# Kernel tuning notes

Measured on AMD Instinct MI355X. Metric: run time of the kernel, lower is better.

Reference implementation:

```python
import jax, jax.numpy as jnp
import numpy as np

VOCAB = 50000
EMB = 512
HID = 1024
B = 256
W = 26


def setup_inputs() -> dict:
    key = jax.random.key(0)
    k0, k1, k2, k3, k4, k5, k6 = jax.random.split(key, 7)
    s = 1.0 / np.sqrt(HID)
    return {
        "ques_vec": jax.random.randint(k0, (B, W), 0, VOCAB + 1, dtype=jnp.int32),
        "ques_len": jax.random.randint(k1, (B,), 1, W + 1, dtype=jnp.int32),
        # nn.Linear(vocab, emb, bias=False).weight -> [emb, vocab]
        "W_emb": jax.random.normal(k2, (EMB, VOCAB), dtype=jnp.float32) * 0.02,
        # PyTorch LSTM params, gate order (i, f, g, o)
        "W_ih": jax.random.uniform(k3, (4 * HID, EMB), jnp.float32, -s, s),
        "W_hh": jax.random.uniform(k4, (4 * HID, HID), jnp.float32, -s, s),
        "b_ih": jax.random.uniform(k5, (4 * HID,), jnp.float32, -s, s),
        "b_hh": jax.random.uniform(k6, (4 * HID,), jnp.float32, -s, s),
    }


def reference(ques_vec, ques_len, W_emb, W_ih, W_hh, b_ih, b_hh):
    # one_hot(vocab+1)[:, :, 1:] @ W_emb.T  ==  gather of W_emb columns;
    # token 0 (pad) maps to the zero embedding.
    tok = ques_vec  # [B, W]
    emb = jnp.where(
        (tok > 0)[..., None],
        W_emb.T[jnp.maximum(tok - 1, 0)],  # [B, W, EMB]
        jnp.zeros((), dtype=W_emb.dtype),
    )
    emb = jnp.tanh(emb)  # tanh(0)=0 for pads, matches torch

    bias = b_ih + b_hh

    def step(carry, xt):
        h, c = carry
        gates = xt @ W_ih.T + h @ W_hh.T + bias  # [B, 4H]
        i, f, g, o = jnp.split(gates, 4, axis=-1)
        c = jax.nn.sigmoid(f) * c + jax.nn.sigmoid(i) * jnp.tanh(g)
        h = jax.nn.sigmoid(o) * jnpp_tanh(c) if False else jax.nn.sigmoid(o) * jnp.tanh(c)
        return (h, c), None

    h0 = jnp.zeros((tok.shape[0], HID), dtype=W_emb.dtype)
    (h_n, _), _ = jax.lax.scan(step, (h0, h0), jnp.swapaxes(emb, 0, 1))
    return h_n  # [B, HID] == h_n.view(B, -1) for 1-layer unidirectional LSTM
```

## Files before the change

### kernel.cpp

```cpp
#include <hip/hip_runtime.h>
#include <hip/hip_bf16.h>

#define VOCAB 50000
#define EMBD  512
#define HID   1024
#define NB    256
#define SEQW  26
#define MTOT  (SEQW * NB)
#define NGATE (4 * HID)

typedef short short8 __attribute__((ext_vector_type(8)));
typedef _Float16 half8 __attribute__((ext_vector_type(8)));
typedef float f32x4  __attribute__((ext_vector_type(4)));
typedef float f32x2  __attribute__((ext_vector_type(2)));

__device__ __forceinline__ unsigned short f16bits(_Float16 h) {
    union { _Float16 h; unsigned short u; } cv; cv.h = h; return cv.u;
}

__device__ __forceinline__ void gload16(const void* g, void* l) {
    __builtin_amdgcn_global_load_lds(
        (const __attribute__((address_space(1))) void*)g,
        (__attribute__((address_space(3))) void*)l, 16, 0, 0);
}

__global__ void init_kernel(unsigned short* __restrict__ hBuf,
                            unsigned int* __restrict__ bar) {
    int idx = blockIdx.x * blockDim.x + threadIdx.x;
    hBuf[idx] = 0;
    if (idx < 4096) bar[idx] = 0;
}

__global__ void transp_kernel(const float* __restrict__ W,
                              unsigned short* __restrict__ WT) {
    __shared__ _Float16 tile[64][72];
    int v0 = blockIdx.x * 64;
    int e0 = blockIdx.y * 64;
    int tid = threadIdx.x;

    int e_loc = tid >> 2, q = tid & 3;
    int vq = q * 16;
    if (v0 + vq < VOCAB) {
        const float* src = W + (size_t)(e0 + e_loc) * VOCAB + v0 + vq;
        #pragma unroll
        for (int j = 0; j < 4; ++j) {
            f32x4 x = *(const f32x4*)(src + 4 * j);
            #pragma unroll
            for (int i = 0; i < 4; ++i)
                tile[vq + 4 * j + i][e_loc] = (_Float16)x[i];
        }
    }
    __syncthreads();

    int v_loc = tid >> 2;
    int ec = q * 16;
    int v = v0 + v_loc;
    if (v < VOCAB) {
        short8* dst = (short8*)(WT + (size_t)v * EMBD + e0 + ec);
        dst[0] = *(const short8*)&tile[v_loc][ec];
        dst[1] = *(const short8*)&tile[v_loc][ec + 8];
    }
}

__global__ void embed_kernel(const int* __restrict__ qv,
                             const unsigned short* __restrict__ WT,
                             unsigned short* __restrict__ eHi) {
    int pair = blockIdx.x * 4 + (threadIdx.x >> 6);
    int t = pair >> 8, b = pair & 255;
    int lane = threadIdx.x & 63;
    int tok = qv[b * SEQW + t];
    short8 out = {};
    if (tok > 0) {
        short8 v = *(const short8*)(WT + (size_t)(tok - 1) * EMBD + lane * 8);
        #pragma unroll
        for (int i = 0; i < 8; ++i) {
            union { short s; _Float16 h; } cv; cv.s = v[i];
            out[i] = (short)f16bits((_Float16)tanhf((float)cv.h));
        }
    }
    *(short8*)(eHi + (size_t)pair * EMBD + lane * 8) = out;
}

__global__ void convw_kernel(const float* __restrict__ Wih,
                             const float* __restrict__ Whh,
                             const float* __restrict__ b_ih,
                             const float* __restrict__ b_hh,
                             unsigned short* __restrict__ ih,
                             unsigned short* __restrict__ hh,
                             float* __restrict__ bsum) {
    int j = blockIdx.x;
    if (threadIdx.x == 0) bsum[j] = b_ih[j] + b_hh[j];
    for (int col = threadIdx.x; col < EMBD; col += blockDim.x)
        ih[(size_t)j * EMBD + col] = f16bits((_Float16)Wih[(size_t)j * EMBD + col]);
    for (int col = threadIdx.x; col < HID; col += blockDim.x)
        hh[(size_t)j * HID + col] = f16bits((_Float16)Whh[(size_t)j * HID + col]);
}

__global__ __launch_bounds__(512, 2) void pregemm_kernel(
    const unsigned short* __restrict__ eHi,
    const unsigned short* __restrict__ ih,
    const float* __restrict__ bsum,
    float* __restrict__ G0n)
{
    __shared__ char smem[65536];

    int id = blockIdx.x;
    int xcd = id & 7, lid = id >> 3;
    int pc = xcd * 4 + (lid & 3);
    int pm = lid >> 2;
    int m0 = pm * 128;

    int tid = threadIdx.x;
    int w = tid >> 6;
    int mh = w >> 2, nh = w & 3;
    int lane = tid & 63;
    int col16 = lane & 15, g4 = lane >> 4;

    int sr = lane >> 3, sc = lane & 7;
    int ra0 = w * 16 + sr, ra1 = ra0 + 8;
    const char* eB = (const char*)eHi;
    const char* iB = (const char*)ih;
    size_t aOffG0 = (size_t)(m0 + ra0) * 1024 + (size_t)(((sc ^ (ra0 & 7))) * 16);
    size_t aOffG1 = (size_t)(m0 + ra1) * 1024 + (size_t)(((sc ^ (ra1 & 7))) * 16);
    int gb0 = (ra0 >> 5) * 1024 + pc * 32 + (ra0 & 31);
    int gb1 = (ra1 >> 5) * 1024 + pc * 32 + (ra1 & 31);
    size_t bOffG0 = (size_t)gb0 * 1024 + (size_t)(((sc ^ (ra0 & 7))) * 16);
    size_t bOffG1 = (size_t)gb1 * 1024 + (size_t)(((sc ^ (ra1 & 7))) * 16);
    int ldsRow0 = (w * 16) * 128;
    int ldsRow1 = (w * 16 + 8) * 128;

    f32x4 acc[4][2];
    #pragma unroll
    for (int fm = 0; fm < 4; ++fm)
        #pragma unroll
        for (int fn = 0; fn < 2; ++fn)
            acc[fm][fn] = (f32x4){0.f, 0.f, 0.f, 0.f};

    int swb = col16 & 7;
    int aRow[4], bRow[2];
    #pragma unroll
    for (int fm = 0; fm < 4; ++fm) aRow[fm] = (mh * 64 + fm * 16 + col16) * 128;
    #pragma unroll
    for (int fn = 0; fn < 2; ++fn) bRow[fn] = (nh * 32 + fn * 16 + col16) * 128;

#define STAGE(kb, buf) do { \
        int kby = (kb) * 128; \
        char* aD = smem + (buf) * 16384; \
        char* bD = smem + 32768 + (buf) * 16384; \
        gload16(eB + aOffG0 + kby, aD + ldsRow0); \
        gload16(eB + aOffG1 + kby, aD + ldsRow1); \
        gload16(iB + bOffG0 + kby, bD + ldsRow0); \
        gload16(iB + bOffG1 + kby, bD + ldsRow1); \
    } while (0)

    STAGE(0, 0);
    #pragma unroll
    for (int kb = 0; kb < 8; ++kb) {
        int cur = kb & 1;
        __syncthreads();
        if (kb < 7) STAGE(kb + 1, cur ^ 1);
        const char* aS = smem + cur * 16384;
        const char* bS = smem + 32768 + cur * 16384;
        #pragma unroll
        for (int kk = 0; kk < 2; ++kk) {
            int co = ((kk * 4 + g4) ^ swb) * 16;
            half8 bF[2];
            #pragma unroll
            for (int fn = 0; fn < 2; ++fn)
                bF[fn] = *(const half8*)(const void*)(bS + bRow[fn] + co);
            #pragma unroll
            for (int fm = 0; fm < 4; ++fm) {
                half8 aF = *(const half8*)(const void*)(aS + aRow[fm] + co);
                #pragma unroll
                for (int fn = 0; fn < 2; ++fn)
                    acc[fm][fn] = __builtin_amdgcn_mfma_f32_16x16x32_f16(
                        aF, bF[fn], acc[fm][fn], 0, 0, 0);
            }
        }
    }
#undef STAGE

    #pragma unroll
    for (int fn = 0; fn < 2; ++fn) {
        int cp = nh * 32 + fn * 16 + col16;
        int gate = cp >> 5;
        int jh = pc * 32 + (cp & 31);
        int ct = jh >> 4, jl = jh & 15;
        int cidx = gate * 16 + jl;
        float bv = bsum[gate * HID + jh];
        #pragma unroll
        for (int fm = 0; fm < 4; ++fm)
            #pragma unroll
            for (int r = 0; r < 4; ++r) {
                int row = m0 + mh * 64 + fm * 16 + g4 * 4 + r;
                int t = row >> 8, b = row & 255;
                G0n[(((size_t)t * 64 + ct) * 256 + b) * 64 + cidx] =
                    acc[fm][fn][r] + bv;
            }
    }
}

__global__ __launch_bounds__(512, 2) void lstm_persist(
    const unsigned short* __restrict__ hh,
    unsigned short* __restrict__ hBuf,
    const float* __restrict__ G0n,
    float* __restrict__ out,
    unsigned int* __restrict__ bar)
{
    extern __shared__ char smem[];
    float* gbuf = (float*)(smem + 65536);

    int bx = blockIdx.x;
    int grp = bx & 7;
    int lid = bx >> 3;
    int m0  = grp * 32;
    int jh0 = lid * 32;

    int tid = threadIdx.x;
    int w = tid >> 6;
    int kq = w >> 2, gate = w & 3;
    int lane = tid & 63;
    int col16 = lane & 15, g4 = lane >> 4;

    unsigned int* flags = bar + grp * 512;

    half8 bB[2][16];
    #pragma unroll
    for (int nf = 0; nf < 2; ++nf) {
        const char* bRow = (const char*)hh +
            (((size_t)(gate * HID + jh0 + nf * 16 + col16)) * HID + kq * 512 + g4 * 8) * 2;
        #pragma unroll
        for (int kk = 0; kk < 16; ++kk)
            bB[nf][kk] = *(const half8*)(const void*)(bRow + kk * 64);
    }

    int srow = tid >> 4, sc = tid & 15;
    int swz = (srow & 7) << 4;
    int swr = (col16 & 7) << 4;
    int ml = srow, jl2 = sc * 2;
    int jh = jh0 + jl2;
    int ctE = jh >> 4, jlE = jh & 15;

    float cReg[2] = {0.f, 0.f};

    for (int t = 0; t < SEQW; ++t) {
        const unsigned short* hIn = hBuf + (size_t)t * NB * HID;
        unsigned short* hOut = hBuf + (size_t)(t + 1) * NB * HID;

        f32x2 g0v[4];
        {
            const float* pg = G0n +
                (((size_t)t * 64 + ctE) * 256 + (m0 + ml)) * 64 + jlE;
            #pragma unroll
            for (int q = 0; q < 4; ++q) g0v[q] = *(const f32x2*)(pg + q * 16);
        }

        f32x4 acc[2][2];
        #pragma unroll
        for (int mf = 0; mf < 2; ++mf)
            #pragma unroll
            for (int nf = 0; nf < 2; ++nf)
                acc[mf][nf] = (f32x4){0.f, 0.f, 0.f, 0.f};

        if (t > 0) {
            {
                const char* hRowB = (const char*)hIn + (size_t)(m0 + srow) * (HID * 2);
                short8 v[8];
                #pragma unroll
                for (int j = 0; j < 8; ++j)
                    v[j] = *(const short8*)(const void*)(hRowB + j * 256 + sc * 16);
                #pragma unroll
                for (int j = 0; j < 8; ++j)
                    *(short8*)(smem + srow * 2048 + ((j * 256 + sc * 16) ^ swz)) = v[j];
            }
            __syncthreads();

            #pragma unroll
            for (int kk = 0; kk < 16; ++kk) {
                int kb = kq * 1024 + kk * 64 + g4 * 16;
                half8 a0 = *(const half8*)(const void*)(smem + col16 * 2048 + (kb ^ swr));
                half8 a1 = *(const half8*)(const void*)(smem + (col16 + 16) * 2048 + (kb ^ swr));
                acc[0][0] = __builtin_amdgcn_mfma_f32_16x16x32_f16(a0, bB[0][kk], acc[0][0], 0, 0, 0);
                acc[0][1] = __builtin_amdgcn_mfma_f32_16x16x32_f16(a0, bB[1][kk], acc[0][1], 0, 0, 0);
                acc[1][0] = __builtin_amdgcn_mfma_f32_16x16x32_f16(a1, bB[0][kk], acc[1][0], 0, 0, 0);
                acc[1][1] = __builtin_amdgcn_mfma_f32_16x16x32_f16(a1, bB[1][kk], acc[1][1], 0, 0, 0);
            }
        }

        #pragma unroll
        for (int mf = 0; mf < 2; ++mf)
            #pragma unroll
            for (int nf = 0; nf < 2; ++nf)
                #pragma unroll
                for (int r = 0; r < 4; ++r)
                    gbuf[(((kq * 4 + gate) * 32) + mf * 16 + g4 * 4 + r) * 36
                         + nf * 16 + col16] = acc[mf][nf][r];
        __syncthreads();

        f32x2 gv[4];
        #pragma unroll
        for (int q = 0; q < 4; ++q) {
            f32x2 p0 = *(const f32x2*)&gbuf[((q) * 32 + ml) * 36 + jl2];
            f32x2 p1 = *(const f32x2*)&gbuf[((4 + q) * 32 + ml) * 36 + jl2];
            gv[q] = p0 + p1;
        }

        float hN[2];
        #pragma unroll
        for (int u = 0; u < 2; ++u) {
            float gi  = gv[0][u] + g0v[0][u];
            float gf  = gv[1][u] + g0v[1][u];
            float gg_ = gv[2][u] + g0v[2][u];
            float go  = gv[3][u] + g0v[3][u];
            float si = 1.0f / (1.0f + expf(-gi));
            float sf = 1.0f / (1.0f + expf(-gf));
            float so = 1.0f / (1.0f + expf(-go));
            float tg = tanhf(gg_);
            float cN = sf * cReg[u] + si * tg;
            hN[u] = so * tanhf(cN);
            cReg[u] = cN;
        }
        size_t p = (size_t)(m0 + ml) * HID + jh;
        if (t == SEQW - 1) {
            *(f32x2*)(out + p) = (f32x2){hN[0], hN[1]};
        } else {
            unsigned int hv = (unsigned int)f16bits((_Float16)hN[0]) |
                              ((unsigned int)f16bits((_Float16)hN[1]) << 16);
            __hip_atomic_store((unsigned int*)(hOut + p), hv,
                               __ATOMIC_RELAXED, __HIP_MEMORY_SCOPE_AGENT);

            __syncthreads();
            unsigned int t1 = (unsigned int)(t + 1);
            if (tid == 0)
                __hip_atomic_store(flags + lid * 16, t1,
                                   __ATOMIC_RELAXED, __HIP_MEMORY_SCOPE_AGENT);
            if (w == 0) {
                for (;;) {
                    unsigned int v = __hip_atomic_load(
                        flags + (lane & 31) * 16, __ATOMIC_RELAXED,
                        __HIP_MEMORY_SCOPE_AGENT);
                    if (__all(v >= t1)) break;
                    __builtin_amdgcn_s_sleep(1);
                }
            }
            __syncthreads();
        }
    }
}

extern "C" void kernel_launch(void* const* d_in, const int* in_sizes, int n_in,
                              void* d_out, int out_size, void* d_ws, size_t ws_size,
                              hipStream_t stream) {
    const int*   qv   = (const int*)d_in[0];
    const float* Wemb = (const float*)d_in[2];
    const float* Wih  = (const float*)d_in[3];
    const float* Whh  = (const float*)d_in[4];
    const float* b_ih = (const float*)d_in[5];
    const float* b_hh = (const float*)d_in[6];
    float* out = (float*)d_out;

    char* ws = (char*)d_ws;
    size_t off = 0;
    unsigned short* eHi  = (unsigned short*)(ws + off); off += (size_t)MTOT * EMBD * 2;
    unsigned short* ih   = (unsigned short*)(ws + off); off += (size_t)NGATE * EMBD * 2;
    unsigned short* hh   = (unsigned short*)(ws + off); off += (size_t)NGATE * HID * 2;
    unsigned short* hBuf = (unsigned short*)(ws + off); off += (size_t)(SEQW + 1) * NB * HID * 2;
    float* bsum          = (float*)(ws + off);          off += (size_t)NGATE * 4;
    unsigned int* bar    = (unsigned int*)(ws + off);   off += 16384;
    off = (off + 255) & ~(size_t)255;
    float* G0n           = (float*)(ws + off);          off += (size_t)MTOT * NGATE * 4;
    unsigned short* WembT = (unsigned short*)G0n;

    init_kernel<<<NB * HID / 256, 256, 0, stream>>>(hBuf, bar);
    transp_kernel<<<dim3(782, 8), 256, 0, stream>>>(Wemb, WembT);
    embed_kernel<<<MTOT / 4, 256, 0, stream>>>(qv, WembT, eHi);
    convw_kernel<<<NGATE, 256, 0, stream>>>(Wih, Whh, b_ih, b_hh, ih, hh, bsum);
    pregemm_kernel<<<1664, 512, 0, stream>>>(eHi, ih, bsum, G0n);

    lstm_persist<<<256, 512, 102400, stream>>>(hh, hBuf, G0n, out, bar);
}
```

Before: 209.2 us.

## Fuse input projection into persistent LSTM via concatenated [Whh|Wih] weights

Removes the separate pre-GEMM kernel that computed x@W_ih^T for every timestep into a large fp32 buffer. Each timestep of the persistent kernel now multiplies the concatenated [h, x_t] (K=1536) by register-resident concatenated weights, loading both the hidden state and the embedding row into LDS with direct global-to-LDS loads. The goal is to drop the pre-GEMM launch and the write and read of the gate-preactivation buffer. In exchange, the serial per-step critical path grows by half, and each wave holds more weight registers.

```diff
diff --git a/kernel.cpp b/kernel.cpp
--- a/kernel.cpp
+++ b/kernel.cpp
@@ -8,6 +8,7 @@
 #define SEQW  26
 #define MTOT  (SEQW * NB)
 #define NGATE (4 * HID)
+#define KCAT  1536
 
 typedef short short8 __attribute__((ext_vector_type(8)));
 typedef _Float16 half8 __attribute__((ext_vector_type(8)));
@@ -85,130 +86,27 @@
                              const float* __restrict__ Whh,
                              const float* __restrict__ b_ih,
                              const float* __restrict__ b_hh,
-                             unsigned short* __restrict__ ih,
-                             unsigned short* __restrict__ hh,
+                             unsigned short* __restrict__ Wcat,
                              float* __restrict__ bsum) {
     int j = blockIdx.x;
     if (threadIdx.x == 0) bsum[j] = b_ih[j] + b_hh[j];
+    for (int col = threadIdx.x; col < HID; col += blockDim.x)
+        Wcat[(size_t)j * KCAT + col] = f16bits((_Float16)Whh[(size_t)j * HID + col]);
     for (int col = threadIdx.x; col < EMBD; col += blockDim.x)
-        ih[(size_t)j * EMBD + col] = f16bits((_Float16)Wih[(size_t)j * EMBD + col]);
-    for (int col = threadIdx.x; col < HID; col += blockDim.x)
-        hh[(size_t)j * HID + col] = f16bits((_Float16)Whh[(size_t)j * HID + col]);
-}
-
-__global__ __launch_bounds__(512, 2) void pregemm_kernel(
+        Wcat[(size_t)j * KCAT + HID + col] = f16bits((_Float16)Wih[(size_t)j * EMBD + col]);
+}
+
+__global__ __launch_bounds__(512, 2) void lstm_persist(
+    const unsigned short* __restrict__ Wcat,
+    const float* __restrict__ bsum,
     const unsigned short* __restrict__ eHi,
-    const unsigned short* __restrict__ ih,
-    const float* __restrict__ bsum,
-    float* __restrict__ G0n)
-{
-    __shared__ char smem[65536];
-
-    int id = blockIdx.x;
-    int xcd = id & 7, lid = id >> 3;
-    int pc = xcd * 4 + (lid & 3);
-    int pm = lid >> 2;
-    int m0 = pm * 128;
-
-    int tid = threadIdx.x;
-    int w = tid >> 6;
-    int mh = w >> 2, nh = w & 3;
-    int lane = tid & 63;
-    int col16 = lane & 15, g4 = lane >> 4;
-
-    int sr = lane >> 3, sc = lane & 7;
-    int ra0 = w * 16 + sr, ra1 = ra0 + 8;
-    const char* eB = (const char*)eHi;
-    const char* iB = (const char*)ih;
-    size_t aOffG0 = (size_t)(m0 + ra0) * 1024 + (size_t)(((sc ^ (ra0 & 7))) * 16);
-    size_t aOffG1 = (size_t)(m0 + ra1) * 1024 + (size_t)(((sc ^ (ra1 & 7))) * 16);
-    int gb0 = (ra0 >> 5) * 1024 + pc * 32 + (ra0 & 31);
-    int gb1 = (ra1 >> 5) * 1024 + pc * 32 + (ra1 & 31);
-    size_t bOffG0 = (size_t)gb0 * 1024 + (size_t)(((sc ^ (ra0 & 7))) * 16);
-    size_t bOffG1 = (size_t)gb1 * 1024 + (size_t)(((sc ^ (ra1 & 7))) * 16);
-    int ldsRow0 = (w * 16) * 128;
-    int ldsRow1 = (w * 16 + 8) * 128;
-
-    f32x4 acc[4][2];
-    #pragma unroll
-    for (int fm = 0; fm < 4; ++fm)
-        #pragma unroll
-        for (int fn = 0; fn < 2; ++fn)
-            acc[fm][fn] = (f32x4){0.f, 0.f, 0.f, 0.f};
-
-    int swb = col16 & 7;
-    int aRow[4], bRow[2];
-    #pragma unroll
-    for (int fm = 0; fm < 4; ++fm) aRow[fm] = (mh * 64 + fm * 16 + col16) * 128;
-    #pragma unroll
-    for (int fn = 0; fn < 2; ++fn) bRow[fn] = (nh * 32 + fn * 16 + col16) * 128;
-
-#define STAGE(kb, buf) do { \
-        int kby = (kb) * 128; \
-        char* aD = smem + (buf) * 16384; \
-        char* bD = smem + 32768 + (buf) * 16384; \
-        gload16(eB + aOffG0 + kby, aD + ldsRow0); \
-        gload16(eB + aOffG1 + kby, aD + ldsRow1); \
-        gload16(iB + bOffG0 + kby, bD + ldsRow0); \
-        gload16(iB + bOffG1 + kby, bD + ldsRow1); \
-    } while (0)
-
-    STAGE(0, 0);
-    #pragma unroll
-    for (int kb = 0; kb < 8; ++kb) {
-        int cur = kb & 1;
-        __syncthreads();
-        if (kb < 7) STAGE(kb + 1, cur ^ 1);
-        const char* aS = smem + cur * 16384;
-        const char* bS = smem + 32768 + cur * 16384;
-        #pragma unroll
-        for (int kk = 0; kk < 2; ++kk) {
-            int co = ((kk * 4 + g4) ^ swb) * 16;
-            half8 bF[2];
-            #pragma unroll
-            for (int fn = 0; fn < 2; ++fn)
-                bF[fn] = *(const half8*)(const void*)(bS + bRow[fn] + co);
-            #pragma unroll
-            for (int fm = 0; fm < 4; ++fm) {
-                half8 aF = *(const half8*)(const void*)(aS + aRow[fm] + co);
-                #pragma unroll
-                for (int fn = 0; fn < 2; ++fn)
-                    acc[fm][fn] = __builtin_amdgcn_mfma_f32_16x16x32_f16(
-                        aF, bF[fn], acc[fm][fn], 0, 0, 0);
-            }
-        }
-    }
-#undef STAGE
-
-    #pragma unroll
-    for (int fn = 0; fn < 2; ++fn) {
-        int cp = nh * 32 + fn * 16 + col16;
-        int gate = cp >> 5;
-        int jh = pc * 32 + (cp & 31);
-        int ct = jh >> 4, jl = jh & 15;
-        int cidx = gate * 16 + jl;
-        float bv = bsum[gate * HID + jh];
-        #pragma unroll
-        for (int fm = 0; fm < 4; ++fm)
-            #pragma unroll
-            for (int r = 0; r < 4; ++r) {
-                int row = m0 + mh * 64 + fm * 16 + g4 * 4 + r;
-                int t = row >> 8, b = row & 255;
-                G0n[(((size_t)t * 64 + ct) * 256 + b) * 64 + cidx] =
-                    acc[fm][fn][r] + bv;
-            }
-    }
-}
-
-__global__ __launch_bounds__(512, 2) void lstm_persist(
-    const unsigned short* __restrict__ hh,
     unsigned short* __restrict__ hBuf,
-    const float* __restrict__ G0n,
     float* __restrict__ out,
     unsigned int* __restrict__ bar)
 {
     extern __shared__ char smem[];
-    float* gbuf = (float*)(smem + 65536);
+    float* gbuf = (float*)smem;
+    float* bsL  = (float*)(smem + 98304);
 
     int bx = blockIdx.x;
     int grp = bx & 7;
@@ -218,104 +116,107 @@
 
     int tid = threadIdx.x;
     int w = tid >> 6;
-    int kq = w >> 2, gate = w & 3;
+    int kq = w & 3, ch = w >> 2;
     int lane = tid & 63;
     int col16 = lane & 15, g4 = lane >> 4;
 
     unsigned int* flags = bar + grp * 512;
 
-    half8 bB[2][16];
+    half8 bB[4][12];
     #pragma unroll
-    for (int nf = 0; nf < 2; ++nf) {
-        const char* bRow = (const char*)hh +
-            (((size_t)(gate * HID + jh0 + nf * 16 + col16)) * HID + kq * 512 + g4 * 8) * 2;
-        #pragma unroll
-        for (int kk = 0; kk < 16; ++kk)
+    for (int nf = 0; nf < 4; ++nf) {
+        int colp = ch * 64 + nf * 16 + col16;
+        int gate = colp >> 5, c32 = colp & 31;
+        const char* bRow = (const char*)Wcat +
+            ((size_t)(gate * HID + jh0 + c32) * KCAT + kq * 384 + g4 * 8) * 2;
+        #pragma unroll
+        for (int kk = 0; kk < 12; ++kk)
             bB[nf][kk] = *(const half8*)(const void*)(bRow + kk * 64);
     }
 
-    int srow = tid >> 4, sc = tid & 15;
-    int swz = (srow & 7) << 4;
-    int swr = (col16 & 7) << 4;
-    int ml = srow, jl2 = sc * 2;
+    if (tid < 128) {
+        int gate = tid >> 5, c32 = tid & 31;
+        bsL[tid] = bsum[gate * HID + jh0 + c32];
+    }
+
+    int ml = tid >> 4, sc = tid & 15, jl2 = sc * 2;
     int jh = jh0 + jl2;
-    int ctE = jh >> 4, jlE = jh & 15;
-
     float cReg[2] = {0.f, 0.f};
+    __syncthreads();
 
     for (int t = 0; t < SEQW; ++t) {
         const unsigned short* hIn = hBuf + (size_t)t * NB * HID;
         unsigned short* hOut = hBuf + (size_t)(t + 1) * NB * HID;
 
-        f32x2 g0v[4];
-        {
-            const float* pg = G0n +
-                (((size_t)t * 64 + ctE) * 256 + (m0 + ml)) * 64 + jlE;
-            #pragma unroll
-            for (int q = 0; q < 4; ++q) g0v[q] = *(const f32x2*)(pg + q * 16);
-        }
-
-        f32x4 acc[2][2];
+        #pragma unroll
+        for (int j = 0; j < 12; ++j) {
+            int row = w * 4 + j / 3;
+            const int third = j % 3;
+            int c = third * 64 + lane;
+            int cs = c ^ (row & 7);
+            const char* src;
+            if (third < 2)
+                src = (const char*)hIn + (size_t)(m0 + row) * 2048 + cs * 16;
+            else
+                src = (const char*)eHi +
+                      (size_t)(t * 256 + m0 + row) * 1024 + (cs - 128) * 16;
+            gload16(src, smem + (w * 12 + j) * 1024);
+        }
+        __syncthreads();
+
+        f32x4 acc[2][4];
         #pragma unroll
         for (int mf = 0; mf < 2; ++mf)
             #pragma unroll
-            for (int nf = 0; nf < 2; ++nf)
+            for (int nf = 0; nf < 4; ++nf)
                 acc[mf][nf] = (f32x4){0.f, 0.f, 0.f, 0.f};
 
-        if (t > 0) {
-            {
-                const char* hRowB = (const char*)hIn + (size_t)(m0 + srow) * (HID * 2);
-                short8 v[8];
+        int swr = (col16 & 7) << 4;
+        #pragma unroll
+        for (int kk = 0; kk < 12; ++kk) {
+            int kb = kq * 768 + kk * 64 + g4 * 16;
+            int kbs = kb ^ swr;
+            half8 a0 = *(const half8*)(const void*)(smem + col16 * 3072 + kbs);
+            half8 a1 = *(const half8*)(const void*)(smem + (col16 + 16) * 3072 + kbs);
+            #pragma unroll
+            for (int nf = 0; nf < 4; ++nf) {
+                acc[0][nf] = __builtin_amdgcn_mfma_f32_16x16x32_f16(a0, bB[nf][kk], acc[0][nf], 0, 0, 0);
+                acc[1][nf] = __builtin_amdgcn_mfma_f32_16x16x32_f16(a1, bB[nf][kk], acc[1][nf], 0, 0, 0);
+            }
+        }
+        __syncthreads();
+
+        #pragma unroll
+        for (int mf = 0; mf < 2; ++mf)
+            #pragma unroll
+            for (int nf = 0; nf < 4; ++nf) {
+                int colp = ch * 64 + nf * 16 + col16;
                 #pragma unroll
-                for (int j = 0; j < 8; ++j)
-                    v[j] = *(const short8*)(const void*)(hRowB + j * 256 + sc * 16);
-                #pragma unroll
-                for (int j = 0; j < 8; ++j)
-                    *(short8*)(smem + srow * 2048 + ((j * 256 + sc * 16) ^ swz)) = v[j];
+                for (int r = 0; r < 4; ++r) {
+                    int row = mf * 16 + g4 * 4 + r;
+                    gbuf[(kq * 32 + row) * 132 + colp] = acc[mf][nf][r];
+                }
             }
-            __syncthreads();
-
-            #pragma unroll
-            for (int kk = 0; kk < 16; ++kk) {
-                int kb = kq * 1024 + kk * 64 + g4 * 16;
-                half8 a0 = *(const half8*)(const void*)(smem + col16 * 2048 + (kb ^ swr));
-                half8 a1 = *(const half8*)(const void*)(smem + (col16 + 16) * 2048 + (kb ^ swr));
-                acc[0][0] = __builtin_amdgcn_mfma_f32_16x16x32_f16(a0, bB[0][kk], acc[0][0], 0, 0, 0);
-                acc[0][1] = __builtin_amdgcn_mfma_f32_16x16x32_f16(a0, bB[1][kk], acc[0][1], 0, 0, 0);
-                acc[1][0] = __builtin_amdgcn_mfma_f32_16x16x32_f16(a1, bB[0][kk], acc[1][0], 0, 0, 0);
-                acc[1][1] = __builtin_amdgcn_mfma_f32_16x16x32_f16(a1, bB[1][kk], acc[1][1], 0, 0, 0);
-            }
-        }
-
-        #pragma unroll
-        for (int mf = 0; mf < 2; ++mf)
-            #pragma unroll
-            for (int nf = 0; nf < 2; ++nf)
-                #pragma unroll
-                for (int r = 0; r < 4; ++r)
-                    gbuf[(((kq * 4 + gate) * 32) + mf * 16 + g4 * 4 + r) * 36
-                         + nf * 16 + col16] = acc[mf][nf][r];
         __syncthreads();
 
-        f32x2 gv[4];
-        #pragma unroll
-        for (int q = 0; q < 4; ++q) {
-            f32x2 p0 = *(const f32x2*)&gbuf[((q) * 32 + ml) * 36 + jl2];
-            f32x2 p1 = *(const f32x2*)&gbuf[((4 + q) * 32 + ml) * 36 + jl2];
-            gv[q] = p0 + p1;
+        float gv[4][2];
+        #pragma unroll
+        for (int g = 0; g < 4; ++g) {
+            f32x2 s = {0.f, 0.f};
+            #pragma unroll
+            for (int q = 0; q < 4; ++q)
+                s += *(const f32x2*)&gbuf[(q * 32 + ml) * 132 + g * 32 + jl2];
+            gv[g][0] = s[0] + bsL[g * 32 + jl2];
+            gv[g][1] = s[1] + bsL[g * 32 + jl2 + 1];
         }
 
         float hN[2];
         #pragma unroll
         for (int u = 0; u < 2; ++u) {
-            float gi  = gv[0][u] + g0v[0][u];
-            float gf  = gv[1][u] + g0v[1][u];
-            float gg_ = gv[2][u] + g0v[2][u];
-            float go  = gv[3][u] + g0v[3][u];
-            float si = 1.0f / (1.0f + expf(-gi));
-            float sf = 1.0f / (1.0f + expf(-gf));
-            float so = 1.0f / (1.0f + expf(-go));
-            float tg = tanhf(gg_);
+            float si = 1.0f / (1.0f + expf(-gv[0][u]));
+            float sf = 1.0f / (1.0f + expf(-gv[1][u]));
+            float tg = tanhf(gv[2][u]);
+            float so = 1.0f / (1.0f + expf(-gv[3][u]));
             float cN = sf * cReg[u] + si * tg;
             hN[u] = so * tanhf(cN);
             cReg[u] = cN;
@@ -362,20 +263,17 @@
     char* ws = (char*)d_ws;
     size_t off = 0;
     unsigned short* eHi  = (unsigned short*)(ws + off); off += (size_t)MTOT * EMBD * 2;
-    unsigned short* ih   = (unsigned short*)(ws + off); off += (size_t)NGATE * EMBD * 2;
-    unsigned short* hh   = (unsigned short*)(ws + off); off += (size_t)NGATE * HID * 2;
+    unsigned short* Wcat = (unsigned short*)(ws + off); off += (size_t)NGATE * KCAT * 2;
     unsigned short* hBuf = (unsigned short*)(ws + off); off += (size_t)(SEQW + 1) * NB * HID * 2;
     float* bsum          = (float*)(ws + off);          off += (size_t)NGATE * 4;
     unsigned int* bar    = (unsigned int*)(ws + off);   off += 16384;
     off = (off + 255) & ~(size_t)255;
-    float* G0n           = (float*)(ws + off);          off += (size_t)MTOT * NGATE * 4;
-    unsigned short* WembT = (unsigned short*)G0n;
+    unsigned short* WembT = (unsigned short*)(ws + off); off += (size_t)VOCAB * EMBD * 2;
 
     init_kernel<<<NB * HID / 256, 256, 0, stream>>>(hBuf, bar);
     transp_kernel<<<dim3(782, 8), 256, 0, stream>>>(Wemb, WembT);
     embed_kernel<<<MTOT / 4, 256, 0, stream>>>(qv, WembT, eHi);
-    convw_kernel<<<NGATE, 256, 0, stream>>>(Wih, Whh, b_ih, b_hh, ih, hh, bsum);
-    pregemm_kernel<<<1664, 512, 0, stream>>>(eHi, ih, bsum, G0n);
-
-    lstm_persist<<<256, 512, 102400, stream>>>(hh, hBuf, G0n, out, bar);
-}
+    convw_kernel<<<NGATE, 256, 0, stream>>>(Wih, Whh, b_ih, b_hh, Wcat, bsum);
+
+    lstm_persist<<<256, 512, 98816, stream>>>(Wcat, bsum, eHi, hBuf, out, bar);
+}
```

Result: slower. 280.9 us (+34.3%).
